# Optimization experiments

Measured on AMD Instinct MI355X. Metric: run time of the kernel, lower is better.

The kernel has to match this reference:

```python
import jax, jax.numpy as jnp
import numpy as np

VOCAB = 100000
EMBED = 128
BATCH = 65536
NEG = 5


def setup_inputs() -> dict:
    key = jax.random.key(0)
    k1, k2, k3, k4, k5 = jax.random.split(key, 5)
    pos_w = jax.random.randint(k1, (BATCH,), 0, VOCAB)
    pos_v = jax.random.randint(k2, (BATCH,), 0, VOCAB)
    neg_v = jax.random.randint(k3, (BATCH, NEG), 0, VOCAB)
    w_table = jax.random.normal(k4, (VOCAB, EMBED), dtype=jnp.float32) * 0.01
    v_table = jax.random.normal(k5, (VOCAB, EMBED), dtype=jnp.float32) * 0.01
    return {"pos_w": pos_w, "pos_v": pos_v, "neg_v": neg_v,
            "w_table": w_table, "v_table": v_table}


def reference(pos_w, pos_v, neg_v, w_table, v_table):
    # Gathers: [B, E] and [B, K, E]
    w_emb = w_table[pos_w]          # [B, E]
    pos_v_emb = v_table[pos_v]      # [B, E]
    neg_v_emb = v_table[neg_v]      # [B, K, E]

    # Positive score: elementwise dot per row
    score1 = jnp.sum(w_emb * pos_v_emb, axis=1)          # [B]
    score1 = jnp.clip(score1, -10.0, 10.0)
    score1 = jax.nn.log_sigmoid(score1)

    # Negative scores: bmm([B,K,E], [B,E,1]) -> [B,K]
    score2 = jnp.einsum('bke,be->bk', neg_v_emb, w_emb)  # [B, K]
    score2 = jnp.clip(score2, -10.0, 10.0)
    score2 = jax.nn.log_sigmoid(-score2)

    loss = -(jnp.sum(score1) + jnp.sum(score2))
    return loss
```

## Files before the change

kernel.cpp:

```cpp
#include <hip/hip_runtime.h>

#define EMBED 128
#define NEG 5

__global__ __launch_bounds__(256) void sgneg_kernel(
    const int* __restrict__ pos_w,
    const int* __restrict__ pos_v,
    const int* __restrict__ neg_v,
    const float* __restrict__ w_table,
    const float* __restrict__ v_table,
    float* __restrict__ out,
    int batch)
{
    const int lane32 = threadIdx.x & 31;
    const int groupInBlock = threadIdx.x >> 5;
    const int groupsPerBlock = blockDim.x >> 5;
    const int group = blockIdx.x * groupsPerBlock + groupInBlock;
    const int nGroups = gridDim.x * groupsPerBlock;

    float acc = 0.0f;

    for (int b = group; b < batch; b += nGroups) {
        const int iw  = pos_w[b];
        const int ipv = pos_v[b];
        const int in0 = neg_v[b * NEG + 0];
        const int in1 = neg_v[b * NEG + 1];
        const int in2 = neg_v[b * NEG + 2];
        const int in3 = neg_v[b * NEG + 3];
        const int in4 = neg_v[b * NEG + 4];

        const size_t off = (size_t)lane32 * 4;
        const float4 w  = *reinterpret_cast<const float4*>(w_table + (size_t)iw  * EMBED + off);
        const float4 pv = *reinterpret_cast<const float4*>(v_table + (size_t)ipv * EMBED + off);
        const float4 n0 = *reinterpret_cast<const float4*>(v_table + (size_t)in0 * EMBED + off);
        const float4 n1 = *reinterpret_cast<const float4*>(v_table + (size_t)in1 * EMBED + off);
        const float4 n2 = *reinterpret_cast<const float4*>(v_table + (size_t)in2 * EMBED + off);
        const float4 n3 = *reinterpret_cast<const float4*>(v_table + (size_t)in3 * EMBED + off);
        const float4 n4 = *reinterpret_cast<const float4*>(v_table + (size_t)in4 * EMBED + off);

        float d0 = fmaf(w.x, pv.x, fmaf(w.y, pv.y, fmaf(w.z, pv.z, w.w * pv.w)));
        float d1 = fmaf(w.x, n0.x, fmaf(w.y, n0.y, fmaf(w.z, n0.z, w.w * n0.w)));
        float d2 = fmaf(w.x, n1.x, fmaf(w.y, n1.y, fmaf(w.z, n1.z, w.w * n1.w)));
        float d3 = fmaf(w.x, n2.x, fmaf(w.y, n2.y, fmaf(w.z, n2.z, w.w * n2.w)));
        float d4 = fmaf(w.x, n3.x, fmaf(w.y, n3.y, fmaf(w.z, n3.z, w.w * n3.w)));
        float d5 = fmaf(w.x, n4.x, fmaf(w.y, n4.y, fmaf(w.z, n4.z, w.w * n4.w)));

        #pragma unroll
        for (int m = 16; m >= 1; m >>= 1) {
            d0 += __shfl_xor(d0, m, 64);
            d1 += __shfl_xor(d1, m, 64);
            d2 += __shfl_xor(d2, m, 64);
            d3 += __shfl_xor(d3, m, 64);
            d4 += __shfl_xor(d4, m, 64);
            d5 += __shfl_xor(d5, m, 64);
        }

        if (lane32 == 0) {
            float s1 = fminf(10.0f, fmaxf(-10.0f, d0));
            acc += log1pf(__expf(-s1));
            float s;
            s = fminf(10.0f, fmaxf(-10.0f, d1)); acc += log1pf(__expf(s));
            s = fminf(10.0f, fmaxf(-10.0f, d2)); acc += log1pf(__expf(s));
            s = fminf(10.0f, fmaxf(-10.0f, d3)); acc += log1pf(__expf(s));
            s = fminf(10.0f, fmaxf(-10.0f, d4)); acc += log1pf(__expf(s));
            s = fminf(10.0f, fmaxf(-10.0f, d5)); acc += log1pf(__expf(s));
        }
    }

    __shared__ float sacc[8];
    if (lane32 == 0) sacc[groupInBlock] = acc;
    __syncthreads();
    if (threadIdx.x == 0) {
        float t = 0.0f;
        #pragma unroll
        for (int i = 0; i < 8; ++i) t += sacc[i];
        atomicAdd(out, t);
    }
}

extern "C" void kernel_launch(void* const* d_in, const int* in_sizes, int n_in,
                              void* d_out, int out_size, void* d_ws, size_t ws_size,
                              hipStream_t stream) {
    const int*   pos_w   = (const int*)d_in[0];
    const int*   pos_v   = (const int*)d_in[1];
    const int*   neg_v   = (const int*)d_in[2];
    const float* w_table = (const float*)d_in[3];
    const float* v_table = (const float*)d_in[4];
    float* out = (float*)d_out;

    const int batch = in_sizes[0];

    hipMemsetAsync(out, 0, sizeof(float), stream);

    const int blocks = 2048;
    sgneg_kernel<<<blocks, 256, 0, stream>>>(pos_w, pos_v, neg_v,
                                             w_table, v_table, out, batch);
}
```

Before: 151.1 us.

## Use 16-lane row groups, one row per group, parallel loss evaluation

Each batch row is now handled by a 16-lane group in which every lane loads two float4 chunks, in place of a grid-stride loop over 32-lane groups. There is one launch block per 16 rows, so 4096 blocks. Scores go to shared memory, and the clip plus log-sigmoid runs in parallel across 96 threads instead of serially on one lane per group. The aim is more memory loads in flight per lane, with the serial transcendental tail removed. The cost is one atomic per 16 rows and an extra block barrier.

```diff
diff --git a/kernel.cpp b/kernel.cpp
--- a/kernel.cpp
+++ b/kernel.cpp
@@ -2,6 +2,19 @@
 
 #define EMBED 128
 #define NEG 5
+#define ROWS_PER_BLOCK 16
+
+__device__ __forceinline__ float dot8(float4 w0, float4 w1, float4 a0, float4 a1) {
+    float s = w0.x * a0.x;
+    s = fmaf(w0.y, a0.y, s);
+    s = fmaf(w0.z, a0.z, s);
+    s = fmaf(w0.w, a0.w, s);
+    s = fmaf(w1.x, a1.x, s);
+    s = fmaf(w1.y, a1.y, s);
+    s = fmaf(w1.z, a1.z, s);
+    s = fmaf(w1.w, a1.w, s);
+    return s;
+}
 
 __global__ __launch_bounds__(256) void sgneg_kernel(
     const int* __restrict__ pos_w,
@@ -12,15 +25,17 @@
     float* __restrict__ out,
     int batch)
 {
-    const int lane32 = threadIdx.x & 31;
-    const int groupInBlock = threadIdx.x >> 5;
-    const int groupsPerBlock = blockDim.x >> 5;
-    const int group = blockIdx.x * groupsPerBlock + groupInBlock;
-    const int nGroups = gridDim.x * groupsPerBlock;
+    const int tid = threadIdx.x;
+    const int lane16 = tid & 15;
+    const int row = tid >> 4;
+    const int b = blockIdx.x * ROWS_PER_BLOCK + row;
 
-    float acc = 0.0f;
+    __shared__ float scores[6 * ROWS_PER_BLOCK];
+    __shared__ float wsum[4];
 
-    for (int b = group; b < batch; b += nGroups) {
+    float d0 = 0.f, d1 = 0.f, d2 = 0.f, d3 = 0.f, d4 = 0.f, d5 = 0.f;
+
+    if (b < batch) {
         const int iw  = pos_w[b];
         const int ipv = pos_v[b];
         const int in0 = neg_v[b * NEG + 0];
@@ -29,53 +44,79 @@
         const int in3 = neg_v[b * NEG + 3];
         const int in4 = neg_v[b * NEG + 4];
 
-        const size_t off = (size_t)lane32 * 4;
-        const float4 w  = *reinterpret_cast<const float4*>(w_table + (size_t)iw  * EMBED + off);
-        const float4 pv = *reinterpret_cast<const float4*>(v_table + (size_t)ipv * EMBED + off);
-        const float4 n0 = *reinterpret_cast<const float4*>(v_table + (size_t)in0 * EMBED + off);
-        const float4 n1 = *reinterpret_cast<const float4*>(v_table + (size_t)in1 * EMBED + off);
-        const float4 n2 = *reinterpret_cast<const float4*>(v_table + (size_t)in2 * EMBED + off);
-        const float4 n3 = *reinterpret_cast<const float4*>(v_table + (size_t)in3 * EMBED + off);
-        const float4 n4 = *reinterpret_cast<const float4*>(v_table + (size_t)in4 * EMBED + off);
+        const size_t o0 = (size_t)lane16 * 4;
+        const size_t o1 = 64 + (size_t)lane16 * 4;
 
-        float d0 = fmaf(w.x, pv.x, fmaf(w.y, pv.y, fmaf(w.z, pv.z, w.w * pv.w)));
-        float d1 = fmaf(w.x, n0.x, fmaf(w.y, n0.y, fmaf(w.z, n0.z, w.w * n0.w)));
-        float d2 = fmaf(w.x, n1.x, fmaf(w.y, n1.y, fmaf(w.z, n1.z, w.w * n1.w)));
-        float d3 = fmaf(w.x, n2.x, fmaf(w.y, n2.y, fmaf(w.z, n2.z, w.w * n2.w)));
-        float d4 = fmaf(w.x, n3.x, fmaf(w.y, n3.y, fmaf(w.z, n3.z, w.w * n3.w)));
-        float d5 = fmaf(w.x, n4.x, fmaf(w.y, n4.y, fmaf(w.z, n4.z, w.w * n4.w)));
+        const float* wr = w_table + (size_t)iw * EMBED;
+        const float4 w0 = *reinterpret_cast<const float4*>(wr + o0);
+        const float4 w1 = *reinterpret_cast<const float4*>(wr + o1);
 
-        #pragma unroll
-        for (int m = 16; m >= 1; m >>= 1) {
-            d0 += __shfl_xor(d0, m, 64);
-            d1 += __shfl_xor(d1, m, 64);
-            d2 += __shfl_xor(d2, m, 64);
-            d3 += __shfl_xor(d3, m, 64);
-            d4 += __shfl_xor(d4, m, 64);
-            d5 += __shfl_xor(d5, m, 64);
-        }
+        const float* pr = v_table + (size_t)ipv * EMBED;
+        const float* r0 = v_table + (size_t)in0 * EMBED;
+        const float* r1 = v_table + (size_t)in1 * EMBED;
+        const float* r2 = v_table + (size_t)in2 * EMBED;
+        const float* r3 = v_table + (size_t)in3 * EMBED;
+        const float* r4 = v_table + (size_t)in4 * EMBED;
 
-        if (lane32 == 0) {
-            float s1 = fminf(10.0f, fmaxf(-10.0f, d0));
-            acc += log1pf(__expf(-s1));
-            float s;
-            s = fminf(10.0f, fmaxf(-10.0f, d1)); acc += log1pf(__expf(s));
-            s = fminf(10.0f, fmaxf(-10.0f, d2)); acc += log1pf(__expf(s));
-            s = fminf(10.0f, fmaxf(-10.0f, d3)); acc += log1pf(__expf(s));
-            s = fminf(10.0f, fmaxf(-10.0f, d4)); acc += log1pf(__expf(s));
-            s = fminf(10.0f, fmaxf(-10.0f, d5)); acc += log1pf(__expf(s));
+        const float4 p0 = *reinterpret_cast<const float4*>(pr + o0);
+        const float4 p1 = *reinterpret_cast<const float4*>(pr + o1);
+        const float4 a0 = *reinterpret_cast<const float4*>(r0 + o0);
+        const float4 a1 = *reinterpret_cast<const float4*>(r0 + o1);
+        const float4 b0 = *reinterpret_cast<const float4*>(r1 + o0);
+        const float4 b1 = *reinterpret_cast<const float4*>(r1 + o1);
+        const float4 c0 = *reinterpret_cast<const float4*>(r2 + o0);
+        const float4 c1 = *reinterpret_cast<const float4*>(r2 + o1);
+        const float4 e0 = *reinterpret_cast<const float4*>(r3 + o0);
+        const float4 e1 = *reinterpret_cast<const float4*>(r3 + o1);
+        const float4 f0 = *reinterpret_cast<const float4*>(r4 + o0);
+        const float4 f1 = *reinterpret_cast<const float4*>(r4 + o1);
+
+        d0 = dot8(w0, w1, p0, p1);
+        d1 = dot8(w0, w1, a0, a1);
+        d2 = dot8(w0, w1, b0, b1);
+        d3 = dot8(w0, w1, c0, c1);
+        d4 = dot8(w0, w1, e0, e1);
+        d5 = dot8(w0, w1, f0, f1);
+    }
+
+    #pragma unroll
+    for (int m = 8; m >= 1; m >>= 1) {
+        d0 += __shfl_xor(d0, m, 64);
+        d1 += __shfl_xor(d1, m, 64);
+        d2 += __shfl_xor(d2, m, 64);
+        d3 += __shfl_xor(d3, m, 64);
+        d4 += __shfl_xor(d4, m, 64);
+        d5 += __shfl_xor(d5, m, 64);
+    }
+
+    if (lane16 == 0) {
+        scores[0 * ROWS_PER_BLOCK + row] = d0;
+        scores[1 * ROWS_PER_BLOCK + row] = d1;
+        scores[2 * ROWS_PER_BLOCK + row] = d2;
+        scores[3 * ROWS_PER_BLOCK + row] = d3;
+        scores[4 * ROWS_PER_BLOCK + row] = d4;
+        scores[5 * ROWS_PER_BLOCK + row] = d5;
+    }
+    __syncthreads();
+
+    float t = 0.0f;
+    if (tid < 6 * ROWS_PER_BLOCK) {
+        const int k = tid >> 4;
+        const int r = tid & 15;
+        const int gb = blockIdx.x * ROWS_PER_BLOCK + r;
+        if (gb < batch) {
+            float s = scores[tid];
+            s = fminf(10.0f, fmaxf(-10.0f, s));
+            const float arg = (k == 0) ? -s : s;
+            t = __logf(1.0f + __expf(arg));
         }
     }
 
-    __shared__ float sacc[8];
-    if (lane32 == 0) sacc[groupInBlock] = acc;
+    #pragma unroll
+    for (int m = 32; m >= 1; m >>= 1) t += __shfl_xor(t, m, 64);
+    if ((tid & 63) == 0) wsum[tid >> 6] = t;
     __syncthreads();
-    if (threadIdx.x == 0) {
-        float t = 0.0f;
-        #pragma unroll
-        for (int i = 0; i < 8; ++i) t += sacc[i];
-        atomicAdd(out, t);
-    }
+    if (tid == 0) atomicAdd(out, wsum[0] + wsum[1] + wsum[2] + wsum[3]);
 }
 
 extern "C" void kernel_launch(void* const* d_in, const int* in_sizes, int n_in,
@@ -92,7 +133,7 @@
 
     hipMemsetAsync(out, 0, sizeof(float), stream);
 
-    const int blocks = 2048;
+    const int blocks = (batch + ROWS_PER_BLOCK - 1) / ROWS_PER_BLOCK;
     sgneg_kernel<<<blocks, 256, 0, stream>>>(pos_w, pos_v, neg_v,
                                              w_table, v_table, out, batch);
 }
```

Result: slower. 167.1 us (+10.6%).
